# Performance work log

Measured on AMD Instinct MI355X. Metric: run time of the kernel, lower is better.

Reference implementation:

```python
import jax, jax.numpy as jnp
import numpy as np

N, D, H = 4_000_000, 10, 16

def setup_inputs() -> dict:
    key = jax.random.key(0)
    k1, k2, k3, k4, k5 = jax.random.split(key, 5)
    x = jax.random.normal(k1, (N, D), dtype=jnp.float32)
    # torch nn.Linear default init: U(-1/sqrt(fan_in), 1/sqrt(fan_in))
    lim1 = 1.0 / np.sqrt(D)
    lim2 = 1.0 / np.sqrt(H)
    W1 = jax.random.uniform(k2, (H, D), dtype=jnp.float32, minval=-lim1, maxval=lim1)
    b1 = jax.random.uniform(k3, (H,), dtype=jnp.float32, minval=-lim1, maxval=lim1)
    W2 = jax.random.uniform(k4, (1, H), dtype=jnp.float32, minval=-lim2, maxval=lim2)
    b2 = jax.random.uniform(k5, (1,), dtype=jnp.float32, minval=-lim2, maxval=lim2)
    return {"x": x, "W1": W1, "b1": b1, "W2": W2, "b2": b2}

def reference(x, W1, b1, W2, b2):
    gram = x.T @ x                      # [10,10] symmetric Gram matrix
    v, w = jnp.linalg.eigh(gram)        # eigenvalues ascending; w: [10,10]
    y = jnp.maximum(w @ W1.T + b1, 0.0) # fc1 + ReLU -> [10,16]
    y = y @ W2.T + b2                   # fc2 -> [10,1]
    return 0.5 * (jax.nn.sigmoid(y) + 1.0)
```

## Files before the change

### kernel.cpp

```cpp
#include <hip/hip_runtime.h>
#include <math.h>


#define BLK2 256
#define GRID2 1024
#define TILE_F4 (BLK2 * 5)

__global__ void zero_ws_kernel(double* __restrict__ g) {
  int t = threadIdx.x;
  if (t < 220) g[t] = 0.0;
}

__global__ __launch_bounds__(BLK2) void gram_kernel(const float4* __restrict__ x4,
                                                    double* __restrict__ g,
                                                    int nf4) {
  __shared__ float4 tile[TILE_F4];
  float acc[55];
#pragma unroll
  for (int k = 0; k < 55; k++) acc[k] = 0.0f;

  const int tid = threadIdx.x;
  const int ntiles = (nf4 + TILE_F4 - 1) / TILE_F4;

  for (int t = blockIdx.x; t < ntiles; t += GRID2) {
    const int base = t * TILE_F4;
    float4 r0, r1, r2, r3, r4;
    {
      int i0 = base + 0 * BLK2 + tid;
      int i1 = base + 1 * BLK2 + tid;
      int i2 = base + 2 * BLK2 + tid;
      int i3 = base + 3 * BLK2 + tid;
      int i4 = base + 4 * BLK2 + tid;
      float4 zz = make_float4(0.f, 0.f, 0.f, 0.f);
      r0 = (i0 < nf4) ? x4[i0] : zz;
      r1 = (i1 < nf4) ? x4[i1] : zz;
      r2 = (i2 < nf4) ? x4[i2] : zz;
      r3 = (i3 < nf4) ? x4[i3] : zz;
      r4 = (i4 < nf4) ? x4[i4] : zz;
    }
    __syncthreads();
    tile[0 * BLK2 + tid] = r0;
    tile[1 * BLK2 + tid] = r1;
    tile[2 * BLK2 + tid] = r2;
    tile[3 * BLK2 + tid] = r3;
    tile[4 * BLK2 + tid] = r4;
    __syncthreads();
    float4 q0 = tile[tid * 5 + 0];
    float4 q1 = tile[tid * 5 + 1];
    float4 q2 = tile[tid * 5 + 2];
    float4 q3 = tile[tid * 5 + 3];
    float4 q4 = tile[tid * 5 + 4];
    float v[20] = {q0.x, q0.y, q0.z, q0.w, q1.x, q1.y, q1.z, q1.w,
                   q2.x, q2.y, q2.z, q2.w, q3.x, q3.y, q3.z, q3.w,
                   q4.x, q4.y, q4.z, q4.w};
    int k = 0;
#pragma unroll
    for (int i = 0; i < 10; i++) {
#pragma unroll
      for (int j = 0; j <= i; j++) {
        acc[k] += v[i] * v[j] + v[10 + i] * v[10 + j];
        k++;
      }
    }
  }

  __shared__ double sred[4][55];
  int lane = threadIdx.x & 63;
  int wv = threadIdx.x >> 6;
#pragma unroll
  for (int k = 0; k < 55; k++) {
    double d = (double)acc[k];
#pragma unroll
    for (int off = 32; off > 0; off >>= 1) d += __shfl_down(d, off, 64);
    if (lane == 0) sred[wv][k] = d;
  }
  __syncthreads();
  double* gr = g + 55 * (blockIdx.x & 3);
  if (threadIdx.x < 55) {
    double s = sred[0][threadIdx.x] + sred[1][threadIdx.x] +
               sred[2][threadIdx.x] + sred[3][threadIdx.x];
    atomicAdd(&gr[threadIdx.x], s);
  }
}


__device__ __forceinline__ float sf_sign(float a, float b) {
  return (b >= 0.0f) ? fabsf(a) : -fabsf(a);
}

__device__ __forceinline__ float slapy2(float x, float y) {
  float xa = fabsf(x), ya = fabsf(y);
  float w = fmaxf(xa, ya), z = fminf(xa, ya);
  if (z == 0.0f) return w;
  float q = z / w;
  return w * sqrtf(1.0f + q * q);
}

__device__ __forceinline__ void slartg(float f, float g, float* c, float* s, float* r) {
  if (g == 0.0f) {
    *c = 1.0f; *s = 0.0f; *r = f;
  } else if (f == 0.0f) {
    *c = 0.0f; *s = sf_sign(1.0f, g); *r = fabsf(g);
  } else {
    float d = sqrtf(f * f + g * g);
    *c = fabsf(f) / d;
    float rr = sf_sign(d, f);
    *s = g / rr;
    *r = rr;
  }
}

__device__ __forceinline__ void slaev2(float a, float b, float c,
                                       float* rt1, float* rt2, float* cs1, float* sn1) {
  float sm = a + c;
  float df = a - c;
  float adf = fabsf(df);
  float tb = b + b;
  float ab = fabsf(tb);
  float acmx, acmn;
  if (fabsf(a) > fabsf(c)) { acmx = a; acmn = c; } else { acmx = c; acmn = a; }
  float rt;
  if (adf > ab)      { float t = ab / adf; rt = adf * sqrtf(1.0f + t * t); }
  else if (adf < ab) { float t = adf / ab; rt = ab * sqrtf(1.0f + t * t); }
  else               { rt = ab * sqrtf(2.0f); }
  int sgn1;
  if (sm < 0.0f) {
    *rt1 = 0.5f * (sm - rt); sgn1 = -1;
    *rt2 = (acmx / *rt1) * acmn - (b / *rt1) * b;
  } else if (sm > 0.0f) {
    *rt1 = 0.5f * (sm + rt); sgn1 = 1;
    *rt2 = (acmx / *rt1) * acmn - (b / *rt1) * b;
  } else {
    *rt1 = 0.5f * rt; *rt2 = -0.5f * rt; sgn1 = 1;
  }
  int sgn2;
  float cs;
  if (df >= 0.0f) { cs = df + rt; sgn2 = 1; } else { cs = df - rt; sgn2 = -1; }
  float acs = fabsf(cs);
  if (acs > ab) {
    float ct = -tb / cs;
    *sn1 = 1.0f / sqrtf(1.0f + ct * ct);
    *cs1 = ct * (*sn1);
  } else {
    if (ab == 0.0f) { *cs1 = 1.0f; *sn1 = 0.0f; }
    else {
      float tn = -cs / tb;
      *cs1 = 1.0f / sqrtf(1.0f + tn * tn);
      *sn1 = tn * (*cs1);
    }
  }
  if (sgn1 == sgn2) { float tn = *cs1; *cs1 = -(*sn1); *sn1 = tn; }
}

__device__ __forceinline__ float sel10(const float* a, int idx0) {
  float v = 0.0f;
#pragma unroll
  for (int k = 0; k < 10; k++) v = (k == idx0) ? a[k] : v;
  return v;
}
__device__ __forceinline__ void put10(float* a, int idx0, float v) {
#pragma unroll
  for (int k = 0; k < 10; k++) a[k] = (k == idx0) ? v : a[k];
}

#define A_(r, c) Am[((r)-1) * 10 + ((c)-1)]
#define Z_(r, c) Zm[((r)-1) * 10 + ((c)-1)]
#define D_(i) dv[(i)-1]
#define E_(i) ev[(i)-1]
#define TAUV(i) tauv[(i)-1]
#define WV(i) wvv[(i)-1]

__global__ __launch_bounds__(64, 1) void eig_mlp_kernel(
    const double* __restrict__ g,
    const float* __restrict__ W1,
    const float* __restrict__ b1,
    const float* __restrict__ W2,
    const float* __restrict__ b2,
    float* __restrict__ out) {
  if (blockIdx.x != 0) return;
  const int lane = threadIdx.x;
  const int n = 10;
  float Am[100], Zm[100];
  float dv[10], ev[10], tauv[10], wvv[10], csv[10], snv[10];

  {
    int k = 0;
#pragma unroll
    for (int i = 0; i < 10; i++)
#pragma unroll
      for (int j = 0; j <= i; j++) {
        double v = g[k] + g[55 + k] + g[110 + k] + g[165 + k];
        float f = (float)v;
        Am[i * 10 + j] = f;
        Am[j * 10 + i] = f;
        k++;
      }
  }

#pragma unroll
  for (int i = 1; i <= n - 1; i++) {
    const int nmi = n - i;
    float alpha = A_(i + 1, i);
    float taui = 0.0f;
    if (nmi > 1) {
      float ss = 0.0f;
#pragma unroll
      for (int r = i + 2; r <= n; r++) { float t = A_(r, i); ss += t * t; }
      float xnorm = sqrtf(ss);
      if (xnorm != 0.0f) {
        float beta = -sf_sign(slapy2(alpha, xnorm), alpha);
        taui = (beta - alpha) / beta;
        float sc = 1.0f / (alpha - beta);
#pragma unroll
        for (int r = i + 2; r <= n; r++) A_(r, i) *= sc;
        alpha = beta;
      }
    }
    E_(i) = alpha;
    A_(i + 1, i) = alpha;
    if (taui != 0.0f) {
      A_(i + 1, i) = 1.0f;
#pragma unroll
      for (int r = i + 1; r <= n; r++) {
        float s = 0.0f;
#pragma unroll
        for (int c = i + 1; c <= n; c++) {
          float arc = (r >= c) ? A_(r, c) : A_(c, r);
          s += arc * A_(c, i);
        }
        WV(r) = taui * s;
      }
      float dot = 0.0f;
#pragma unroll
      for (int r = i + 1; r <= n; r++) dot += WV(r) * A_(r, i);
      float al2 = -0.5f * taui * dot;
#pragma unroll
      for (int r = i + 1; r <= n; r++) WV(r) += al2 * A_(r, i);
#pragma unroll
      for (int c = i + 1; c <= n; c++)
#pragma unroll
        for (int r = c; r <= n; r++)
          A_(r, c) -= A_(r, i) * WV(c) + WV(r) * A_(c, i);
      A_(i + 1, i) = E_(i);
    }
    D_(i) = A_(i, i);
    TAUV(i) = taui;
  }
  D_(n) = A_(n, n);

#pragma unroll
  for (int r = 1; r <= n; r++)
#pragma unroll
    for (int c = 1; c <= n; c++) Z_(r, c) = (r == c) ? 1.0f : 0.0f;
#pragma unroll
  for (int i = n - 1; i >= 1; i--) {
    float taui = TAUV(i);
    if (taui != 0.0f) {
#pragma unroll
      for (int c = 1; c <= n; c++) {
        float t = Z_(i + 1, c);
#pragma unroll
        for (int r = i + 2; r <= n; r++) t += A_(r, i) * Z_(r, c);
        t *= taui;
        Z_(i + 1, c) -= t;
#pragma unroll
        for (int r = i + 2; r <= n; r++) Z_(r, c) -= A_(r, i) * t;
      }
    }
  }

  const int r_own = (lane < 10) ? lane : 0;
  float z[10];
#pragma unroll
  for (int k = 0; k < 10; k++) {
    float v = Zm[0 * 10 + k];
#pragma unroll
    for (int rr = 1; rr < 10; rr++) v = (r_own == rr) ? Zm[rr * 10 + k] : v;
    z[k] = v;
  }

  const float eps = 5.9604644775390625e-08f;
  const float eps2 = eps * eps;
  const float safmin = 1.17549435082228751e-38f;
  const int nmaxit = n * 30;
  int jtot = 0;
  int l1 = 1;
  int guard = 0;

  while (l1 <= n && guard++ < 2000) {
    if (l1 > 1) put10(ev, l1 - 2, 0.0f);
    int m = n;
    {
      bool found = false;
#pragma unroll
      for (int k = 1; k <= n - 1; k++) {
        if (!found && k >= l1) {
          float tst = fabsf(ev[k - 1]);
          if (tst == 0.0f) {
            m = k; found = true;
          } else if (tst <= (sqrtf(fabsf(dv[k - 1])) * sqrtf(fabsf(dv[k]))) * eps) {
            ev[k - 1] = 0.0f;
            m = k; found = true;
          }
        }
      }
    }
    int l = l1, lsv = l, lend = m, lendsv = m;
    l1 = m + 1;
    if (lend == l) continue;
    if (fabsf(sel10(dv, lend - 1)) < fabsf(sel10(dv, l - 1))) { lend = lsv; l = lendsv; }

    if (lend > l) {
      for (;;) {
        if (guard++ > 4000) break;
        int m2 = lend;
        if (l != lend) {
          bool fnd = false;
#pragma unroll
          for (int k = 1; k <= n - 1; k++) {
            if (!fnd && k >= l && k <= lend - 1) {
              float e = ev[k - 1];
              if (e * e <= (eps2 * fabsf(dv[k - 1])) * fabsf(dv[k]) + safmin) {
                m2 = k; fnd = true;
              }
            }
          }
        }
        if (m2 < lend) put10(ev, m2 - 1, 0.0f);
        float p = sel10(dv, l - 1);
        if (m2 == l) {
          put10(dv, l - 1, p);
          l = l + 1;
          if (l <= lend) continue;
          break;
        }
        if (m2 == l + 1) {
          float rt1, rt2, c2, s2;
          slaev2(sel10(dv, l - 1), sel10(ev, l - 1), sel10(dv, l), &rt1, &rt2, &c2, &s2);
          float a = sel10(z, l);
          float b = sel10(z, l - 1);
          put10(z, l, c2 * a - s2 * b);
          put10(z, l - 1, s2 * a + c2 * b);
          put10(dv, l - 1, rt1);
          put10(dv, l, rt2);
          put10(ev, l - 1, 0.0f);
          l = l + 2;
          if (l <= lend) continue;
          break;
        }
        if (jtot == nmaxit) break;
        jtot++;
        float El = sel10(ev, l - 1);
        float gg = (sel10(dv, l) - p) / (2.0f * El);
        float rr = slapy2(gg, 1.0f);
        gg = sel10(dv, m2 - 1) - p + (El / (gg + sf_sign(rr, gg)));
        float s = 1.0f, c = 1.0f;
        p = 0.0f;
#pragma unroll
        for (int i = n - 1; i >= 1; i--) {
          if (i <= m2 - 1 && i >= l) {
            float e = ev[i - 1];
            float f = s * e, b = c * e;
            slartg(gg, f, &c, &s, &rr);
            if (i != m2 - 1) ev[i] = rr;
            gg = dv[i] - p;
            rr = (dv[i - 1] - gg) * s + 2.0f * c * b;
            p = s * rr;
            dv[i] = gg + p;
            gg = c * rr - b;
            csv[i - 1] = c;
            snv[i - 1] = -s;
          }
        }
        {
          float a = sel10(z, m2 - 1);
#pragma unroll
          for (int j = n - 1; j >= 1; j--) {
            if (j <= m2 - 1 && j >= l) {
              float cj = csv[j - 1], sj = snv[j - 1];
              float b = z[j - 1];
              z[j] = cj * a - sj * b;
              a = sj * a + cj * b;
            }
          }
          put10(z, l - 1, a);
        }
        put10(dv, l - 1, sel10(dv, l - 1) - p);
        put10(ev, l - 1, gg);
      }
    } else {
      for (;;) {
        if (guard++ > 4000) break;
        int m2 = lend;
        if (l != lend) {
          bool fnd = false;
#pragma unroll
          for (int k = n; k >= 2; k--) {
            if (!fnd && k <= l && k >= lend + 1) {
              float e = ev[k - 2];
              if (e * e <= (eps2 * fabsf(dv[k - 1])) * fabsf(dv[k - 2]) + safmin) {
                m2 = k; fnd = true;
              }
            }
          }
        }
        if (m2 > lend) put10(ev, m2 - 2, 0.0f);
        float p = sel10(dv, l - 1);
        if (m2 == l) {
          put10(dv, l - 1, p);
          l = l - 1;
          if (l >= lend) continue;
          break;
        }
        if (m2 == l - 1) {
          float rt1, rt2, c2, s2;
          slaev2(sel10(dv, l - 2), sel10(ev, l - 2), sel10(dv, l - 1), &rt1, &rt2, &c2, &s2);
          float a = sel10(z, l - 1);
          float b = sel10(z, l - 2);
          put10(z, l - 1, c2 * a - s2 * b);
          put10(z, l - 2, s2 * a + c2 * b);
          put10(dv, l - 2, rt1);
          put10(dv, l - 1, rt2);
          put10(ev, l - 2, 0.0f);
          l = l - 2;
          if (l >= lend) continue;
          break;
        }
        if (jtot == nmaxit) break;
        jtot++;
        float El1 = sel10(ev, l - 2);
        float gg = (sel10(dv, l - 2) - p) / (2.0f * El1);
        float rr = slapy2(gg, 1.0f);
        gg = sel10(dv, m2 - 1) - p + (El1 / (gg + sf_sign(rr, gg)));
        float s = 1.0f, c = 1.0f;
        p = 0.0f;
#pragma unroll
        for (int i = 1; i <= n - 1; i++) {
          if (i >= m2 && i <= l - 1) {
            float e = ev[i - 1];
            float f = s * e, b = c * e;
            slartg(gg, f, &c, &s, &rr);
            if (i >= 2) {
              if (i != m2) ev[i - 2] = rr;
            }
            gg = dv[i - 1] - p;
            rr = (dv[i] - gg) * s + 2.0f * c * b;
            p = s * rr;
            dv[i - 1] = gg + p;
            gg = c * rr - b;
            csv[i - 1] = c;
            snv[i - 1] = s;
          }
        }
        {
          float carry = sel10(z, m2 - 1);
#pragma unroll
          for (int j = 1; j <= n - 1; j++) {
            if (j >= m2 && j <= l - 1) {
              float cj = csv[j - 1], sj = snv[j - 1];
              float t = z[j];
              z[j - 1] = sj * t + cj * carry;
              carry = cj * t - sj * carry;
            }
          }
          put10(z, l - 1, carry);
        }
        put10(dv, l - 1, sel10(dv, l - 1) - p);
        put10(ev, l - 2, gg);
      }
    }
  }

  for (int ii = 2; ii <= n; ii++) {
    int i = ii - 1;
    int k = i;
    float p = sel10(dv, i - 1);
    for (int j = ii; j <= n; j++) {
      float dj = sel10(dv, j - 1);
      if (dj < p) { k = j; p = dj; }
    }
    if (k != i) {
      float di = sel10(dv, i - 1);
      put10(dv, k - 1, di);
      put10(dv, i - 1, p);
      float a = sel10(z, i - 1), b = sel10(z, k - 1);
      put10(z, i - 1, b);
      put10(z, k - 1, a);
    }
  }

  if (lane < 10) {
    double o = (double)b2[0];
#pragma unroll
    for (int h = 0; h < 16; h++) {
      double sgm = (double)b1[h];
#pragma unroll
      for (int k = 0; k < 10; k++) sgm += (double)z[k] * (double)W1[h * 10 + k];
      if (sgm > 0.0) o += sgm * (double)W2[h];
    }
    double sig = 1.0 / (1.0 + exp(-o));
    out[lane] = (float)(0.5 * (sig + 1.0));
  }
}

extern "C" void kernel_launch(void* const* d_in, const int* in_sizes, int n_in,
                              void* d_out, int out_size, void* d_ws, size_t ws_size,
                              hipStream_t stream) {
  const float* x  = (const float*)d_in[0];
  const float* W1 = (const float*)d_in[1];
  const float* b1 = (const float*)d_in[2];
  const float* W2 = (const float*)d_in[3];
  const float* b2 = (const float*)d_in[4];
  double* g = (double*)d_ws;
  float* out = (float*)d_out;

  int nf4 = in_sizes[0] / 4;

  zero_ws_kernel<<<1, 256, 0, stream>>>(g);
  gram_kernel<<<GRID2, BLK2, 0, stream>>>((const float4*)x, g, nf4);
  eig_mlp_kernel<<<1, 64, 0, stream>>>(g, W1, b1, W2, b2, out);
}
```

Before: 339.5 us.

## Load Gram tiles per wave via direct global-to-LDS DMA and make eigensolver branches wave-uniform

The Gram kernel now gives each wave its own 320-float4 LDS tile, filled with global_load_lds (direct global-to-LDS DMA) instead of loading into registers, storing to LDS and hitting block barriers. This removes the two __syncthreads per tile and the register staging, and occupancy is raised with launch_bounds(256,4). In the eigensolver, data-dependent branch conditions are made wave-uniform with readfirstlane, so the compiler can emit scalar branches instead of divergent masks. The per-wave tiling drops the tail when nf4 is not a multiple of 320 (it happens to divide here), and relying on lane 0 assumes all lanes hold identical values.

```diff
diff --git a/kernel.cpp b/kernel.cpp
--- a/kernel.cpp
+++ b/kernel.cpp
@@ -4,52 +4,45 @@
 
 #define BLK2 256
 #define GRID2 1024
-#define TILE_F4 (BLK2 * 5)
+#define WTILE 320
+#define NWAVES (GRID2 * 4)
+
+typedef const __attribute__((address_space(1))) void* gas_ptr;
+typedef __attribute__((address_space(3))) void* las_ptr;
+
+__device__ __forceinline__ void load_lds16(const void* g, void* l) {
+  __builtin_amdgcn_global_load_lds((gas_ptr)g, (las_ptr)l, 16, 0, 0);
+}
 
 __global__ void zero_ws_kernel(double* __restrict__ g) {
   int t = threadIdx.x;
   if (t < 220) g[t] = 0.0;
 }
 
-__global__ __launch_bounds__(BLK2) void gram_kernel(const float4* __restrict__ x4,
-                                                    double* __restrict__ g,
-                                                    int nf4) {
-  __shared__ float4 tile[TILE_F4];
+__global__ __launch_bounds__(BLK2, 4) void gram_kernel(const float4* __restrict__ x4,
+                                                       double* __restrict__ g,
+                                                       int nf4) {
+  __shared__ float4 tile[4 * WTILE];
   float acc[55];
 #pragma unroll
   for (int k = 0; k < 55; k++) acc[k] = 0.0f;
 
-  const int tid = threadIdx.x;
-  const int ntiles = (nf4 + TILE_F4 - 1) / TILE_F4;
-
-  for (int t = blockIdx.x; t < ntiles; t += GRID2) {
-    const int base = t * TILE_F4;
-    float4 r0, r1, r2, r3, r4;
-    {
-      int i0 = base + 0 * BLK2 + tid;
-      int i1 = base + 1 * BLK2 + tid;
-      int i2 = base + 2 * BLK2 + tid;
-      int i3 = base + 3 * BLK2 + tid;
-      int i4 = base + 4 * BLK2 + tid;
-      float4 zz = make_float4(0.f, 0.f, 0.f, 0.f);
-      r0 = (i0 < nf4) ? x4[i0] : zz;
-      r1 = (i1 < nf4) ? x4[i1] : zz;
-      r2 = (i2 < nf4) ? x4[i2] : zz;
-      r3 = (i3 < nf4) ? x4[i3] : zz;
-      r4 = (i4 < nf4) ? x4[i4] : zz;
-    }
-    __syncthreads();
-    tile[0 * BLK2 + tid] = r0;
-    tile[1 * BLK2 + tid] = r1;
-    tile[2 * BLK2 + tid] = r2;
-    tile[3 * BLK2 + tid] = r3;
-    tile[4 * BLK2 + tid] = r4;
-    __syncthreads();
-    float4 q0 = tile[tid * 5 + 0];
-    float4 q1 = tile[tid * 5 + 1];
-    float4 q2 = tile[tid * 5 + 2];
-    float4 q3 = tile[tid * 5 + 3];
-    float4 q4 = tile[tid * 5 + 4];
+  const int lane = threadIdx.x & 63;
+  const int wv = threadIdx.x >> 6;
+  const int gwave = blockIdx.x * 4 + wv;
+  const int nwt = nf4 / WTILE;
+  float4* lbase = &tile[wv * WTILE];
+
+  for (int t = gwave; t < nwt; t += NWAVES) {
+    const float4* gsrc = x4 + (size_t)t * WTILE + lane;
+#pragma unroll
+    for (int k = 0; k < 5; k++) load_lds16(gsrc + k * 64, lbase + k * 64);
+    __builtin_amdgcn_s_waitcnt(0);
+    float4 q0 = lbase[lane * 5 + 0];
+    float4 q1 = lbase[lane * 5 + 1];
+    float4 q2 = lbase[lane * 5 + 2];
+    float4 q3 = lbase[lane * 5 + 3];
+    float4 q4 = lbase[lane * 5 + 4];
     float v[20] = {q0.x, q0.y, q0.z, q0.w, q1.x, q1.y, q1.z, q1.w,
                    q2.x, q2.y, q2.z, q2.w, q3.x, q3.y, q3.z, q3.w,
                    q4.x, q4.y, q4.z, q4.w};
@@ -65,8 +58,6 @@
   }
 
   __shared__ double sred[4][55];
-  int lane = threadIdx.x & 63;
-  int wv = threadIdx.x >> 6;
 #pragma unroll
   for (int k = 0; k < 55; k++) {
     double d = (double)acc[k];
@@ -84,6 +75,10 @@
 }
 
 
+__device__ __forceinline__ int u_cond(bool b) {
+  return __builtin_amdgcn_readfirstlane(b ? 1 : 0);
+}
+
 __device__ __forceinline__ float sf_sign(float a, float b) {
   return (b >= 0.0f) ? fabsf(a) : -fabsf(a);
 }
@@ -91,15 +86,16 @@
 __device__ __forceinline__ float slapy2(float x, float y) {
   float xa = fabsf(x), ya = fabsf(y);
   float w = fmaxf(xa, ya), z = fminf(xa, ya);
-  if (z == 0.0f) return w;
+  if (u_cond(z == 0.0f)) return w;
   float q = z / w;
   return w * sqrtf(1.0f + q * q);
 }
 
 __device__ __forceinline__ void slartg(float f, float g, float* c, float* s, float* r) {
-  if (g == 0.0f) {
+  int cls = __builtin_amdgcn_readfirstlane(g == 0.0f ? 0 : (f == 0.0f ? 1 : 2));
+  if (cls == 0) {
     *c = 1.0f; *s = 0.0f; *r = f;
-  } else if (f == 0.0f) {
+  } else if (cls == 1) {
     *c = 0.0f; *s = sf_sign(1.0f, g); *r = fabsf(g);
   } else {
     float d = sqrtf(f * f + g * g);
@@ -118,16 +114,17 @@
   float tb = b + b;
   float ab = fabsf(tb);
   float acmx, acmn;
-  if (fabsf(a) > fabsf(c)) { acmx = a; acmn = c; } else { acmx = c; acmn = a; }
+  if (u_cond(fabsf(a) > fabsf(c))) { acmx = a; acmn = c; } else { acmx = c; acmn = a; }
   float rt;
-  if (adf > ab)      { float t = ab / adf; rt = adf * sqrtf(1.0f + t * t); }
-  else if (adf < ab) { float t = adf / ab; rt = ab * sqrtf(1.0f + t * t); }
-  else               { rt = ab * sqrtf(2.0f); }
+  if (u_cond(adf > ab))      { float t = ab / adf; rt = adf * sqrtf(1.0f + t * t); }
+  else if (u_cond(adf < ab)) { float t = adf / ab; rt = ab * sqrtf(1.0f + t * t); }
+  else                       { rt = ab * sqrtf(2.0f); }
   int sgn1;
-  if (sm < 0.0f) {
+  int smc = __builtin_amdgcn_readfirstlane(sm < 0.0f ? 0 : (sm > 0.0f ? 1 : 2));
+  if (smc == 0) {
     *rt1 = 0.5f * (sm - rt); sgn1 = -1;
     *rt2 = (acmx / *rt1) * acmn - (b / *rt1) * b;
-  } else if (sm > 0.0f) {
+  } else if (smc == 1) {
     *rt1 = 0.5f * (sm + rt); sgn1 = 1;
     *rt2 = (acmx / *rt1) * acmn - (b / *rt1) * b;
   } else {
@@ -135,14 +132,14 @@
   }
   int sgn2;
   float cs;
-  if (df >= 0.0f) { cs = df + rt; sgn2 = 1; } else { cs = df - rt; sgn2 = -1; }
+  if (u_cond(df >= 0.0f)) { cs = df + rt; sgn2 = 1; } else { cs = df - rt; sgn2 = -1; }
   float acs = fabsf(cs);
-  if (acs > ab) {
+  if (u_cond(acs > ab)) {
     float ct = -tb / cs;
     *sn1 = 1.0f / sqrtf(1.0f + ct * ct);
     *cs1 = ct * (*sn1);
   } else {
-    if (ab == 0.0f) { *cs1 = 1.0f; *sn1 = 0.0f; }
+    if (u_cond(ab == 0.0f)) { *cs1 = 1.0f; *sn1 = 0.0f; }
     else {
       float tn = -cs / tb;
       *cs1 = 1.0f / sqrtf(1.0f + tn * tn);
@@ -207,7 +204,7 @@
 #pragma unroll
       for (int r = i + 2; r <= n; r++) { float t = A_(r, i); ss += t * t; }
       float xnorm = sqrtf(ss);
-      if (xnorm != 0.0f) {
+      if (u_cond(xnorm != 0.0f)) {
         float beta = -sf_sign(slapy2(alpha, xnorm), alpha);
         taui = (beta - alpha) / beta;
         float sc = 1.0f / (alpha - beta);
@@ -218,7 +215,7 @@
     }
     E_(i) = alpha;
     A_(i + 1, i) = alpha;
-    if (taui != 0.0f) {
+    if (u_cond(taui != 0.0f)) {
       A_(i + 1, i) = 1.0f;
 #pragma unroll
       for (int r = i + 1; r <= n; r++) {
@@ -255,7 +252,7 @@
 #pragma unroll
   for (int i = n - 1; i >= 1; i--) {
     float taui = TAUV(i);
-    if (taui != 0.0f) {
+    if (u_cond(taui != 0.0f)) {
 #pragma unroll
       for (int c = 1; c <= n; c++) {
         float t = Z_(i + 1, c);
@@ -290,38 +287,37 @@
   while (l1 <= n && guard++ < 2000) {
     if (l1 > 1) put10(ev, l1 - 2, 0.0f);
     int m = n;
-    {
-      bool found = false;
-#pragma unroll
-      for (int k = 1; k <= n - 1; k++) {
-        if (!found && k >= l1) {
-          float tst = fabsf(ev[k - 1]);
-          if (tst == 0.0f) {
-            m = k; found = true;
-          } else if (tst <= (sqrtf(fabsf(dv[k - 1])) * sqrtf(fabsf(dv[k]))) * eps) {
-            ev[k - 1] = 0.0f;
-            m = k; found = true;
-          }
+#pragma unroll
+    for (int k = 1; k <= n - 1; k++) {
+      if (m == n && k >= l1) {
+        float tst = fabsf(ev[k - 1]);
+        int cls = __builtin_amdgcn_readfirstlane(
+            tst == 0.0f
+                ? 1
+                : (tst <= (sqrtf(fabsf(dv[k - 1])) * sqrtf(fabsf(dv[k]))) * eps ? 2 : 0));
+        if (cls) {
+          if (cls == 2) ev[k - 1] = 0.0f;
+          m = k;
         }
       }
     }
     int l = l1, lsv = l, lend = m, lendsv = m;
     l1 = m + 1;
     if (lend == l) continue;
-    if (fabsf(sel10(dv, lend - 1)) < fabsf(sel10(dv, l - 1))) { lend = lsv; l = lendsv; }
+    if (u_cond(fabsf(sel10(dv, lend - 1)) < fabsf(sel10(dv, l - 1)))) { lend = lsv; l = lendsv; }
 
     if (lend > l) {
       for (;;) {
         if (guard++ > 4000) break;
         int m2 = lend;
         if (l != lend) {
-          bool fnd = false;
+          int fnd = 0;
 #pragma unroll
           for (int k = 1; k <= n - 1; k++) {
             if (!fnd && k >= l && k <= lend - 1) {
               float e = ev[k - 1];
-              if (e * e <= (eps2 * fabsf(dv[k - 1])) * fabsf(dv[k]) + safmin) {
-                m2 = k; fnd = true;
+              if (u_cond(e * e <= (eps2 * fabsf(dv[k - 1])) * fabsf(dv[k]) + safmin)) {
+                m2 = k; fnd = 1;
               }
             }
           }
@@ -393,13 +389,13 @@
         if (guard++ > 4000) break;
         int m2 = lend;
         if (l != lend) {
-          bool fnd = false;
+          int fnd = 0;
 #pragma unroll
           for (int k = n; k >= 2; k--) {
             if (!fnd && k <= l && k >= lend + 1) {
               float e = ev[k - 2];
-              if (e * e <= (eps2 * fabsf(dv[k - 1])) * fabsf(dv[k - 2]) + safmin) {
-                m2 = k; fnd = true;
+              if (u_cond(e * e <= (eps2 * fabsf(dv[k - 1])) * fabsf(dv[k - 2]) + safmin)) {
+                m2 = k; fnd = 1;
               }
             }
           }
@@ -477,7 +473,7 @@
     float p = sel10(dv, i - 1);
     for (int j = ii; j <= n; j++) {
       float dj = sel10(dv, j - 1);
-      if (dj < p) { k = j; p = dj; }
+      if (u_cond(dj < p)) { k = j; p = dj; }
     }
     if (k != i) {
       float di = sel10(dv, i - 1);
```

Result: slower. 373.6 us (+10.0%).
